# Optimization experiments

Measured on AMD Instinct MI355X. Metric: run time of the kernel, lower is better.

## Reference

```python
import jax, jax.numpy as jnp
import numpy as np

KH = KW = 3  # kernel_size

def _extract_patches(x):
    # x: [B, C, H, W] -> patches [B, C, Ho, Wo, KH*KW], same ordering as nn.Unfold
    B, C, H, W = x.shape
    Ho, Wo = H - KH + 1, W - KW + 1
    slices = [x[:, :, i:i + Ho, j:j + Wo] for i in range(KH) for j in range(KW)]
    return jnp.stack(slices, axis=-1)

def setup_inputs() -> dict:
    key = jax.random.key(0)
    k1, k2 = jax.random.split(key)
    x = jax.random.normal(k1, (16, 64, 128, 128), dtype=jnp.float32)
    W = jax.random.normal(k2, (8, KH * KW), dtype=jnp.float32) * (1.0 / np.sqrt(KH * KW))
    return {"x": x, "W": W}

def reference(x, W):
    # per-patch: out = Linear(SiLU(patch)) for each of n_convs kernels and each channel
    B, C, H, Wd = x.shape
    Ho, Wo = H - KH + 1, Wd - KW + 1
    patches = _extract_patches(x)                      # [B, C, Ho, Wo, 9]
    act = jax.nn.silu(patches)
    # out channel ordering: kern + channel * n_convs -> [B, C, K, Ho, Wo]
    out = jnp.einsum('bchwj,kj->bckhw', act, W)
    return out.reshape(B, C * W.shape[0], Ho, Wo)
```

## Files before the change

kernel.cpp:

```cpp
#include <hip/hip_runtime.h>

#define B_   16
#define C_   64
#define H_   128
#define W_   128
#define HO   126
#define WO   126
#define NK   8
#define ROWS 14
#define INR  16

__global__ __launch_bounds__(512) void conv_silu_kernel(
    const float* __restrict__ x, const float* __restrict__ Wt,
    float* __restrict__ out)
{
    __shared__ float s[INR][W_];

    const int band = blockIdx.x;
    const int c    = blockIdx.y;
    const int b    = blockIdx.z;
    const int tid  = threadIdx.x;
    const int ho0  = band * ROWS;

    {
        const float4* xv =
            (const float4*)(x + ((size_t)(b * C_ + c) * H_ + ho0) * W_);
        const float4 v = xv[tid];
        const int row = tid >> 5;
        const int col = (tid & 31) << 2;
        float4 sv;
        sv.x = v.x * __builtin_amdgcn_rcpf(1.0f + __expf(-v.x));
        sv.y = v.y * __builtin_amdgcn_rcpf(1.0f + __expf(-v.y));
        sv.z = v.z * __builtin_amdgcn_rcpf(1.0f + __expf(-v.z));
        sv.w = v.w * __builtin_amdgcn_rcpf(1.0f + __expf(-v.w));
        *(float4*)&s[row][col] = sv;
    }
    __syncthreads();

    const int l  = tid & 63;
    const int ws = __builtin_amdgcn_readfirstlane((int)(threadIdx.x >> 6));

    float w9[9];
#pragma unroll
    for (int j = 0; j < 9; ++j) w9[j] = Wt[ws * 9 + j];

    float* op = out + ((size_t)((b * C_ + c) * NK + ws) * HO + ho0) * WO;

    float tA[3][3], tB[3][3];
#pragma unroll
    for (int j = 0; j < 3; ++j) {
#pragma unroll
        for (int d = 0; d < 3; ++d) {
            tA[j][d] = s[j][l + d];
            tB[j][d] = s[j][(64 + l + d) & 127];
        }
    }

#pragma unroll
    for (int r = 0; r < ROWS; ++r) {
        float accA = 0.f, accB = 0.f;
#pragma unroll
        for (int j = 0; j < 3; ++j) {
#pragma unroll
            for (int d = 0; d < 3; ++d) {
                const float ww = w9[j * 3 + d];
                accA += ww * tA[j][d];
                accB += ww * tB[j][d];
            }
        }
        op[r * WO + l] = accA;
        if (l < 62) op[r * WO + 64 + l] = accB;

        if (r < ROWS - 1) {
#pragma unroll
            for (int j = 0; j < 2; ++j) {
#pragma unroll
                for (int d = 0; d < 3; ++d) {
                    tA[j][d] = tA[j + 1][d];
                    tB[j][d] = tB[j + 1][d];
                }
            }
#pragma unroll
            for (int d = 0; d < 3; ++d) {
                tA[2][d] = s[r + 3][l + d];
                tB[2][d] = s[r + 3][(64 + l + d) & 127];
            }
        }
    }
}

extern "C" void kernel_launch(void* const* d_in, const int* in_sizes, int n_in,
                              void* d_out, int out_size, void* d_ws, size_t ws_size,
                              hipStream_t stream) {
    const float* x  = (const float*)d_in[0];
    const float* Wt = (const float*)d_in[1];
    float* out = (float*)d_out;

    dim3 grid(9, C_, B_);
    conv_silu_kernel<<<grid, 512, 0, stream>>>(x, Wt, out);
}
```

Before: 116.6 us.

## Make blocks persistent over row bands with double-buffered LDS prefetch

Each block now handles one (batch, channel) plane and loops over all nine row bands instead of launching one block per band. The next band's input is loaded into registers before the current band is computed, then SiLU'd and written into the other LDS buffer afterwards, so global loads overlap compute and stores. This cuts the grid size ninefold, which lowers parallelism and may reduce latency hiding on a memory-bound kernel. Each band still reloads its two halo rows from global memory.

```diff
diff --git a/kernel.cpp b/kernel.cpp
--- a/kernel.cpp
+++ b/kernel.cpp
@@ -9,82 +9,100 @@
 #define NK   8
 #define ROWS 14
 #define INR  16
+#define NB   9
 
 __global__ __launch_bounds__(512) void conv_silu_kernel(
     const float* __restrict__ x, const float* __restrict__ Wt,
     float* __restrict__ out)
 {
-    __shared__ float s[INR][W_];
+    __shared__ float s[2][INR][W_];
 
-    const int band = blockIdx.x;
-    const int c    = blockIdx.y;
-    const int b    = blockIdx.z;
-    const int tid  = threadIdx.x;
-    const int ho0  = band * ROWS;
+    const int c   = blockIdx.x;
+    const int b   = blockIdx.y;
+    const int tid = threadIdx.x;
+    const int row = tid >> 5;
+    const int col = (tid & 31) << 2;
+
+    const float* xp = x + (size_t)(b * C_ + c) * H_ * W_;
+
+    const int l  = tid & 63;
+    const int ws = __builtin_amdgcn_readfirstlane((int)(threadIdx.x >> 6));
+    float w9[9];
+#pragma unroll
+    for (int j = 0; j < 9; ++j) w9[j] = Wt[ws * 9 + j];
 
     {
-        const float4* xv =
-            (const float4*)(x + ((size_t)(b * C_ + c) * H_ + ho0) * W_);
-        const float4 v = xv[tid];
-        const int row = tid >> 5;
-        const int col = (tid & 31) << 2;
+        const float4 v = ((const float4*)xp)[tid];
         float4 sv;
         sv.x = v.x * __builtin_amdgcn_rcpf(1.0f + __expf(-v.x));
         sv.y = v.y * __builtin_amdgcn_rcpf(1.0f + __expf(-v.y));
         sv.z = v.z * __builtin_amdgcn_rcpf(1.0f + __expf(-v.z));
         sv.w = v.w * __builtin_amdgcn_rcpf(1.0f + __expf(-v.w));
-        *(float4*)&s[row][col] = sv;
-    }
-    __syncthreads();
-
-    const int l  = tid & 63;
-    const int ws = __builtin_amdgcn_readfirstlane((int)(threadIdx.x >> 6));
-
-    float w9[9];
-#pragma unroll
-    for (int j = 0; j < 9; ++j) w9[j] = Wt[ws * 9 + j];
-
-    float* op = out + ((size_t)((b * C_ + c) * NK + ws) * HO + ho0) * WO;
-
-    float tA[3][3], tB[3][3];
-#pragma unroll
-    for (int j = 0; j < 3; ++j) {
-#pragma unroll
-        for (int d = 0; d < 3; ++d) {
-            tA[j][d] = s[j][l + d];
-            tB[j][d] = s[j][(64 + l + d) & 127];
-        }
+        *(float4*)&s[0][row][col] = sv;
     }
 
-#pragma unroll
-    for (int r = 0; r < ROWS; ++r) {
-        float accA = 0.f, accB = 0.f;
+    float* opb = out + (size_t)((b * C_ + c) * NK + ws) * HO * WO;
+
+    for (int band = 0; band < NB; ++band) {
+        const int cur = band & 1;
+
+        float4 vn;
+        if (band < NB - 1)
+            vn = ((const float4*)(xp + (size_t)(ROWS * (band + 1)) * W_))[tid];
+
+        __syncthreads();
+
+        float* op = opb + (size_t)band * ROWS * WO;
+
+        float tA[3][3], tB[3][3];
 #pragma unroll
         for (int j = 0; j < 3; ++j) {
 #pragma unroll
             for (int d = 0; d < 3; ++d) {
-                const float ww = w9[j * 3 + d];
-                accA += ww * tA[j][d];
-                accB += ww * tB[j][d];
+                tA[j][d] = s[cur][j][l + d];
+                tB[j][d] = s[cur][j][(64 + l + d) & 127];
             }
         }
-        op[r * WO + l] = accA;
-        if (l < 62) op[r * WO + 64 + l] = accB;
 
-        if (r < ROWS - 1) {
 #pragma unroll
-            for (int j = 0; j < 2; ++j) {
+        for (int r = 0; r < ROWS; ++r) {
+            float accA = 0.f, accB = 0.f;
+#pragma unroll
+            for (int j = 0; j < 3; ++j) {
 #pragma unroll
                 for (int d = 0; d < 3; ++d) {
-                    tA[j][d] = tA[j + 1][d];
-                    tB[j][d] = tB[j + 1][d];
+                    const float ww = w9[j * 3 + d];
+                    accA += ww * tA[j][d];
+                    accB += ww * tB[j][d];
                 }
             }
+            op[r * WO + l] = accA;
+            if (l < 62) op[r * WO + 64 + l] = accB;
+
+            if (r < ROWS - 1) {
 #pragma unroll
-            for (int d = 0; d < 3; ++d) {
-                tA[2][d] = s[r + 3][l + d];
-                tB[2][d] = s[r + 3][(64 + l + d) & 127];
+                for (int j = 0; j < 2; ++j) {
+#pragma unroll
+                    for (int d = 0; d < 3; ++d) {
+                        tA[j][d] = tA[j + 1][d];
+                        tB[j][d] = tB[j + 1][d];
+                    }
+                }
+#pragma unroll
+                for (int d = 0; d < 3; ++d) {
+                    tA[2][d] = s[cur][r + 3][l + d];
+                    tB[2][d] = s[cur][r + 3][(64 + l + d) & 127];
+                }
             }
+        }
+
+        if (band < NB - 1) {
+            float4 sv;
+            sv.x = vn.x * __builtin_amdgcn_rcpf(1.0f + __expf(-vn.x));
+            sv.y = vn.y * __builtin_amdgcn_rcpf(1.0f + __expf(-vn.y));
+            sv.z = vn.z * __builtin_amdgcn_rcpf(1.0f + __expf(-vn.z));
+            sv.w = vn.w * __builtin_amdgcn_rcpf(1.0f + __expf(-vn.w));
+            *(float4*)&s[cur ^ 1][row][col] = sv;
         }
     }
 }
@@ -96,6 +114,6 @@
     const float* Wt = (const float*)d_in[1];
     float* out = (float*)d_out;
 
-    dim3 grid(9, C_, B_);
+    dim3 grid(C_, B_);
     conv_silu_kernel<<<grid, 512, 0, stream>>>(x, Wt, out);
 }
```

Measured after the change: 139.5 us. 1.2x slower.

## Drop LDS staging; stream rows from global with register sliding window per half

Applied to the files above, without the earlier changes.

Replaces the shared-memory band tile with direct global loads into a register sliding window. Each block now covers half the output rows for four kernels, and the next input row is prefetched one iteration ahead. This removes the LDS write, the __syncthreads and the LDS reads. In exchange, SiLU is recomputed by every wave, once per kernel (four times per block), and each element is loaded several times from global/L2 with overlapping unaligned reads. Fewer, longer-running blocks also reduce parallelism.

```diff
diff --git a/kernel.cpp b/kernel.cpp
--- a/kernel.cpp
+++ b/kernel.cpp
@@ -7,57 +7,63 @@
 #define HO   126
 #define WO   126
 #define NK   8
-#define ROWS 14
-#define INR  16
+#define HALF 63
 
-__global__ __launch_bounds__(512) void conv_silu_kernel(
+__device__ __forceinline__ float silu_f(float t) {
+    return t * __builtin_amdgcn_rcpf(1.0f + __expf(-t));
+}
+
+__global__ __launch_bounds__(256) void conv_silu_kernel(
     const float* __restrict__ x, const float* __restrict__ Wt,
     float* __restrict__ out)
 {
-    __shared__ float s[INR][W_];
-
-    const int band = blockIdx.x;
+    const int tid  = threadIdx.x;
+    const int l    = tid & 63;
+    const int wv   = tid >> 6;
+    const int half = blockIdx.x & 1;
+    const int kgrp = blockIdx.x >> 1;
     const int c    = blockIdx.y;
     const int b    = blockIdx.z;
-    const int tid  = threadIdx.x;
-    const int ho0  = band * ROWS;
-
-    {
-        const float4* xv =
-            (const float4*)(x + ((size_t)(b * C_ + c) * H_ + ho0) * W_);
-        const float4 v = xv[tid];
-        const int row = tid >> 5;
-        const int col = (tid & 31) << 2;
-        float4 sv;
-        sv.x = v.x * __builtin_amdgcn_rcpf(1.0f + __expf(-v.x));
-        sv.y = v.y * __builtin_amdgcn_rcpf(1.0f + __expf(-v.y));
-        sv.z = v.z * __builtin_amdgcn_rcpf(1.0f + __expf(-v.z));
-        sv.w = v.w * __builtin_amdgcn_rcpf(1.0f + __expf(-v.w));
-        *(float4*)&s[row][col] = sv;
-    }
-    __syncthreads();
-
-    const int l  = tid & 63;
-    const int ws = __builtin_amdgcn_readfirstlane((int)(threadIdx.x >> 6));
+    const int k    = __builtin_amdgcn_readfirstlane(kgrp * 4 + wv);
 
     float w9[9];
 #pragma unroll
-    for (int j = 0; j < 9; ++j) w9[j] = Wt[ws * 9 + j];
+    for (int j = 0; j < 9; ++j) w9[j] = Wt[k * 9 + j];
 
-    float* op = out + ((size_t)((b * C_ + c) * NK + ws) * HO + ho0) * WO;
+    const float* xp = x + (size_t)(b * C_ + c) * H_ * W_;
+    float*       op = out + (size_t)((b * C_ + c) * NK + k) * HO * WO;
+
+    const int r0 = half * HALF;
+
+    const int ca  = l;
+    const int cb0 = (64 + l)     & 127;
+    const int cb1 = (64 + l + 1) & 127;
+    const int cb2 = (64 + l + 2) & 127;
 
     float tA[3][3], tB[3][3];
 #pragma unroll
-    for (int j = 0; j < 3; ++j) {
-#pragma unroll
-        for (int d = 0; d < 3; ++d) {
-            tA[j][d] = s[j][l + d];
-            tB[j][d] = s[j][(64 + l + d) & 127];
-        }
+    for (int j = 0; j < 2; ++j) {
+        const float* rp = xp + (size_t)(r0 + j) * W_;
+        tA[j][0] = silu_f(rp[ca]);  tA[j][1] = silu_f(rp[ca + 1]);  tA[j][2] = silu_f(rp[ca + 2]);
+        tB[j][0] = silu_f(rp[cb0]); tB[j][1] = silu_f(rp[cb1]);     tB[j][2] = silu_f(rp[cb2]);
+    }
+    float pA0, pA1, pA2, pB0, pB1, pB2;
+    {
+        const float* rp = xp + (size_t)(r0 + 2) * W_;
+        pA0 = rp[ca];  pA1 = rp[ca + 1]; pA2 = rp[ca + 2];
+        pB0 = rp[cb0]; pB1 = rp[cb1];    pB2 = rp[cb2];
     }
 
-#pragma unroll
-    for (int r = 0; r < ROWS; ++r) {
+#pragma unroll 3
+    for (int r = 0; r < HALF; ++r) {
+        const int rn = (r0 + r + 3 < H_) ? (r0 + r + 3) : (H_ - 1);
+        const float* rp = xp + (size_t)rn * W_;
+        const float qA0 = rp[ca],  qA1 = rp[ca + 1], qA2 = rp[ca + 2];
+        const float qB0 = rp[cb0], qB1 = rp[cb1],    qB2 = rp[cb2];
+
+        tA[2][0] = silu_f(pA0); tA[2][1] = silu_f(pA1); tA[2][2] = silu_f(pA2);
+        tB[2][0] = silu_f(pB0); tB[2][1] = silu_f(pB1); tB[2][2] = silu_f(pB2);
+
         float accA = 0.f, accB = 0.f;
 #pragma unroll
         for (int j = 0; j < 3; ++j) {
@@ -68,24 +74,18 @@
                 accB += ww * tB[j][d];
             }
         }
-        op[r * WO + l] = accA;
-        if (l < 62) op[r * WO + 64 + l] = accB;
 
-        if (r < ROWS - 1) {
+        float* orow = op + (size_t)(r0 + r) * WO;
+        orow[l] = accA;
+        if (l < 62) orow[64 + l] = accB;
+
 #pragma unroll
-            for (int j = 0; j < 2; ++j) {
-#pragma unroll
-                for (int d = 0; d < 3; ++d) {
-                    tA[j][d] = tA[j + 1][d];
-                    tB[j][d] = tB[j + 1][d];
-                }
-            }
-#pragma unroll
-            for (int d = 0; d < 3; ++d) {
-                tA[2][d] = s[r + 3][l + d];
-                tB[2][d] = s[r + 3][(64 + l + d) & 127];
-            }
+        for (int d = 0; d < 3; ++d) {
+            tA[0][d] = tA[1][d]; tA[1][d] = tA[2][d];
+            tB[0][d] = tB[1][d]; tB[1][d] = tB[2][d];
         }
+        pA0 = qA0; pA1 = qA1; pA2 = qA2;
+        pB0 = qB0; pB1 = qB1; pB2 = qB2;
     }
 }
 
@@ -96,6 +96,6 @@
     const float* Wt = (const float*)d_in[1];
     float* out = (float*)d_out;
 
-    dim3 grid(9, C_, B_);
-    conv_silu_kernel<<<grid, 512, 0, stream>>>(x, Wt, out);
+    dim3 grid(4, C_, B_);
+    conv_silu_kernel<<<grid, 256, 0, stream>>>(x, Wt, out);
 }
```

Result: slower. 221.5 us (+90.0%).
